# Kernel optimization log

Measured on AMD Instinct MI355X. Metric: run time of the kernel, lower is better.

Reference implementation:

```python
import jax, jax.numpy as jnp
import numpy as np

B, T = 256, 512
DX, DZ, DH1, DH2, DDZ, DDX = 100, 100, 10, 10, 20, 20


def _gru_cell(x, h, W_ih, W_hh, b_ih, b_hh):
    # PyTorch GRU cell: gates ordered (r, z, n)
    gi = x @ W_ih.T + b_ih
    gh = h @ W_hh.T + b_hh
    i_r, i_z, i_n = jnp.split(gi, 3, axis=-1)
    h_r, h_z, h_n = jnp.split(gh, 3, axis=-1)
    r = jax.nn.sigmoid(i_r + h_r)
    u = jax.nn.sigmoid(i_z + h_z)
    n = jnp.tanh(i_n + r * h_n)
    return (1.0 - u) * n + u * h


def _mlp(h_in, W1, b1, Wloc, bloc, Wscale, bscale):
    # stoch_trans: relu hidden -> (loc, softplus scale)
    h = jax.nn.relu(h_in @ W1.T + b1)
    return h @ Wloc.T + bloc, jax.nn.softplus(h @ Wscale.T + bscale)


def setup_inputs() -> dict:
    key = jax.random.key(0)
    ks = jax.random.split(key, 22)
    w = lambda k, s: (jax.random.normal(k, s) * 0.1).astype(jnp.float32)
    return dict(
        x=jax.random.normal(ks[0], (B, T, DX), dtype=jnp.float32),
        eps=jax.random.normal(ks[1], (B, T, DZ), dtype=jnp.float32),
        W_ih1=w(ks[2], (3 * DH1, DZ)), W_hh1=w(ks[3], (3 * DH1, DH1)),
        b_ih1=w(ks[4], (3 * DH1,)), b_hh1=w(ks[5], (3 * DH1,)),
        W_ih2=w(ks[6], (3 * DH2, DX)), W_hh2=w(ks[7], (3 * DH2, DH2)),
        b_ih2=w(ks[8], (3 * DH2,)), b_hh2=w(ks[9], (3 * DH2,)),
        dz_W1=w(ks[10], (DDZ, DH1)), dz_b1=w(ks[11], (DDZ,)),
        dz_Wloc=w(ks[12], (DZ, DDZ)), dz_bloc=w(ks[13], (DZ,)),
        dz_Wscale=w(ks[14], (DZ, DDZ)), dz_bscale=w(ks[15], (DZ,)),
        dx_W1=w(ks[16], (DDX, DH1 + DH2)), dx_b1=w(ks[17], (DDX,)),
        dx_Wloc=w(ks[18], (DX, DDX)), dx_bloc=w(ks[19], (DX,)),
        dx_Wscale=w(ks[20], (DX, DDX)), dx_bscale=w(ks[21], (DX,)),
        h1_0=jnp.zeros((DH1,), jnp.float32),
        h2_0=jnp.zeros((DH2,), jnp.float32),
    )


def reference(x, eps, W_ih1, W_hh1, b_ih1, b_hh1, W_ih2, W_hh2, b_ih2, b_hh2,
              dz_W1, dz_b1, dz_Wloc, dz_bloc, dz_Wscale, dz_bscale,
              dx_W1, dx_b1, dx_Wloc, dx_bloc, dx_Wscale, dx_bscale,
              h1_0, h2_0):
    batch = x.shape[0]
    # gen_RNN_2 over the whole observation sequence (no z dependence -> one scan)
    h2_init = jnp.broadcast_to(h2_0, (batch, DH2))
    def step2(h, xt):
        hn = _gru_cell(xt, h, W_ih2, W_hh2, b_ih2, b_hh2)
        return hn, hn
    _, h2_seq = jax.lax.scan(step2, h2_init, jnp.swapaxes(x, 0, 1))  # (T, B, DH2)
    # dx at step t uses h2 after t-1 inputs; first step uses h2_0
    h2_shift = jnp.concatenate([h2_init[None], h2_seq[:-1]], axis=0)

    # sequential generative rollout: dz MLP -> reparam sample -> gen_RNN_1 step -> dx MLP
    h1_init = jnp.broadcast_to(h1_0, (batch, DH1))
    def step(h1, inp):
        eps_t, h2_t = inp
        z_loc, z_scale = _mlp(h1, dz_W1, dz_b1, dz_Wloc, dz_bloc, dz_Wscale, dz_bscale)
        z_t = z_loc + z_scale * eps_t  # reparameterized Normal sample
        h1n = _gru_cell(z_t, h1, W_ih1, W_hh1, b_ih1, b_hh1)
        x_loc, x_scale = _mlp(jnp.concatenate([h1n, h2_t], axis=-1),
                              dx_W1, dx_b1, dx_Wloc, dx_bloc, dx_Wscale, dx_bscale)
        return h1n, (z_t, z_loc, z_scale, x_loc, x_scale)
    _, outs = jax.lax.scan(step, h1_init, (jnp.swapaxes(eps, 0, 1), h2_shift))
    z_t, z_loc, z_scale, x_loc, x_scale = (jnp.swapaxes(o, 0, 1) for o in outs)
    # (B, T, 2*DX + 3*DZ)
    return jnp.concatenate([x_loc, x_scale, z_loc, z_scale, z_t], axis=-1)
```

## Files before the change

### kernel.cpp

```cpp
#include <hip/hip_runtime.h>

#define NB   256
#define NT   512
#define DHX  100
#define DHZ  100
#define DOUT 500
#define WIN  8
#define RING 16

__device__ __forceinline__ float sgm(float v) { return 1.f / (1.f + __expf(-v)); }
__device__ __forceinline__ float tnh(float v) {
    v = fminf(fmaxf(v, -15.f), 15.f);
    float e = __expf(2.f * v);
    return (e - 1.f) / (e + 1.f);
}
__device__ __forceinline__ float sftp(float v) {
    return fmaxf(v, 0.f) + __logf(1.f + __expf(-fabsf(v)));
}
__device__ __forceinline__ float rdlane(float v, int k) {
    return __uint_as_float(__builtin_amdgcn_readlane(__float_as_uint(v), (unsigned)k));
}

__global__ __launch_bounds__(128, 1) void arfssm(
    const float* __restrict__ x, const float* __restrict__ eps,
    const float* __restrict__ W_ih1, const float* __restrict__ W_hh1,
    const float* __restrict__ b_ih1, const float* __restrict__ b_hh1,
    const float* __restrict__ W_ih2, const float* __restrict__ W_hh2,
    const float* __restrict__ b_ih2, const float* __restrict__ b_hh2,
    const float* __restrict__ dz_W1, const float* __restrict__ dz_b1,
    const float* __restrict__ dz_Wloc, const float* __restrict__ dz_bloc,
    const float* __restrict__ dz_Wscale, const float* __restrict__ dz_bscale,
    const float* __restrict__ dx_W1, const float* __restrict__ dx_b1,
    const float* __restrict__ dx_Wloc, const float* __restrict__ dx_bloc,
    const float* __restrict__ dx_Wscale, const float* __restrict__ dx_bscale,
    const float* __restrict__ h1_0, const float* __restrict__ h2_0,
    float* __restrict__ out)
{
    __shared__ __align__(16) float h1d[RING][12];
    __shared__ __align__(16) float xbuf[2][104];
    __shared__ __align__(16) float zbuf[104];

    const int tid = threadIdx.x;
    const int b   = blockIdx.x;

    if (tid < 64) {
        const int l = tid;

        float wdz1[10]; float bdz1 = 0.f;
        #pragma unroll
        for (int k = 0; k < 10; ++k) wdz1[k] = 0.f;
        if (l < 20) {
            #pragma unroll
            for (int k = 0; k < 10; ++k) wdz1[k] = dz_W1[l * 10 + k];
            bdz1 = dz_b1[l];
        }
        float wzl1[20], wzs1[20];
        #pragma unroll
        for (int k = 0; k < 20; ++k) { wzl1[k] = dz_Wloc[l * 20 + k]; wzs1[k] = dz_Wscale[l * 20 + k]; }
        const float bzl1 = dz_bloc[l], bzs1 = dz_bscale[l];
        float wzl2[20], wzs2[20]; float bzl2 = 0.f, bzs2 = 0.f;
        #pragma unroll
        for (int k = 0; k < 20; ++k) { wzl2[k] = 0.f; wzs2[k] = 0.f; }
        if (l < 36) {
            const int j2 = l + 64;
            #pragma unroll
            for (int k = 0; k < 20; ++k) { wzl2[k] = dz_Wloc[j2 * 20 + k]; wzs2[k] = dz_Wscale[j2 * 20 + k]; }
            bzl2 = dz_bloc[j2]; bzs2 = dz_bscale[j2];
        }
        const int gi_i = l >> 1, gi_h = l & 1;
        float wA[52]; float bih_p = 0.f, bhh_p = 0.f; float whh_p[10];
        #pragma unroll
        for (int k = 0; k < 52; ++k) wA[k] = 0.f;
        #pragma unroll
        for (int k = 0; k < 10; ++k) whh_p[k] = 0.f;
        if (l < 60) {
            const int k0 = gi_h ? 52 : 0;
            const int kn = gi_h ? 48 : 52;
            #pragma unroll
            for (int k = 0; k < 52; ++k) if (k < kn) wA[k] = W_ih1[gi_i * 100 + k0 + k];
            bih_p = b_ih1[gi_i];
            bhh_p = b_hh1[gi_i];
            #pragma unroll
            for (int k = 0; k < 10; ++k) whh_p[k] = W_hh1[gi_i * 10 + k];
        }

        float hs[10];
        #pragma unroll
        for (int k = 0; k < 10; ++k) hs[k] = h1_0[k];
        float h1own = (l < 10) ? h1_0[l] : 0.f;
        if (l < 4) zbuf[100 + l] = 0.f;
        float e1c = eps[(size_t)b * NT * DHZ + l];
        float e2c = (l < 36) ? eps[(size_t)b * NT * DHZ + 64 + l] : 0.f;

        for (int w = 0; w < 64; ++w) {
            #pragma unroll 2
            for (int i = 0; i < 8; ++i) {
                const int t   = 8 * w + i;
                const int wsl = (t + 1) & (RING - 1);

                float hv = bdz1;
                #pragma unroll
                for (int k = 0; k < 10; ++k) hv = fmaf(wdz1[k], hs[k], hv);
                hv = fmaxf(hv, 0.f);
                float hd[20];
                #pragma unroll
                for (int k = 0; k < 20; ++k) hd[k] = rdlane(hv, k);

                const int tn = (t + 1 < NT) ? (t + 1) : t;
                const float* ern = eps + ((size_t)b * NT + tn) * DHZ;
                float e1n = ern[l];
                float e2n = (l < 36) ? ern[64 + l] : 0.f;

                float vl1 = bzl1, vs1 = bzs1, vl2 = bzl2, vs2 = bzs2;
                #pragma unroll
                for (int k = 0; k < 20; ++k) {
                    vl1 = fmaf(wzl1[k], hd[k], vl1); vs1 = fmaf(wzs1[k], hd[k], vs1);
                    vl2 = fmaf(wzl2[k], hd[k], vl2); vs2 = fmaf(wzs2[k], hd[k], vs2);
                }
                float sp1 = sftp(vs1), sp2 = sftp(vs2);
                float zt1 = fmaf(sp1, e1c, vl1);
                float zt2 = fmaf(sp2, e2c, vl2);
                zbuf[l] = zt1;
                if (l < 36) zbuf[64 + l] = zt2;
                __builtin_amdgcn_wave_barrier();

                const size_t ob = ((size_t)b * NT + t) * DOUT;
                out[ob + 200 + l] = vl1; out[ob + 300 + l] = sp1; out[ob + 400 + l] = zt1;
                if (l < 36) { out[ob + 264 + l] = vl2; out[ob + 364 + l] = sp2; out[ob + 464 + l] = zt2; }
                e1c = e1n; e2c = e2n;

                const float4* z4 = (const float4*)zbuf;
                const int b4 = gi_h ? 13 : 0;
                float a0 = 0.f, a1 = 0.f, a2 = 0.f, a3 = 0.f;
                #pragma unroll
                for (int q = 0; q < 13; ++q) {
                    float4 zz = z4[b4 + q];
                    a0 = fmaf(wA[4*q+0], zz.x, a0);
                    a1 = fmaf(wA[4*q+1], zz.y, a1);
                    a2 = fmaf(wA[4*q+2], zz.z, a2);
                    a3 = fmaf(wA[4*q+3], zz.w, a3);
                }
                float acc = (a0 + a1) + (a2 + a3);
                acc += __shfl_xor(acc, 1, 64);
                float gh = bhh_p;
                #pragma unroll
                for (int k = 0; k < 10; ++k) gh = fmaf(whh_p[k], hs[k], gh);
                float gih  = acc + bih_p;
                float gsum = gih + gh;

                float s_r  = __shfl(gsum, 2 * l,      64);
                float s_u  = __shfl(gsum, 2 * l + 20, 64);
                float g_in = __shfl(gih,  2 * l + 40, 64);
                float g_hn = __shfl(gh,   2 * l + 40, 64);
                float r = sgm(s_r), u = sgm(s_u);
                float n = tnh(fmaf(r, g_hn, g_in));
                float h1n_v = (1.f - u) * n + u * h1own;

                if (l < 10) h1d[wsl][l] = h1n_v;
                #pragma unroll
                for (int k = 0; k < 10; ++k) hs[k] = rdlane(h1n_v, k);
                h1own = h1n_v;
            }
            __syncthreads();
        }
        __syncthreads();
    } else {
        const int l = tid - 64;

        float wdx1[20]; float bdx1 = 0.f;
        #pragma unroll
        for (int k = 0; k < 20; ++k) wdx1[k] = 0.f;
        if (l < 20) {
            #pragma unroll
            for (int k = 0; k < 20; ++k) wdx1[k] = dx_W1[l * 20 + k];
            bdx1 = dx_b1[l];
        }
        float wxl1[20], wxs1[20];
        #pragma unroll
        for (int k = 0; k < 20; ++k) { wxl1[k] = dx_Wloc[l * 20 + k]; wxs1[k] = dx_Wscale[l * 20 + k]; }
        const float bxl1 = dx_bloc[l], bxs1 = dx_bscale[l];
        float wxl2[20], wxs2[20]; float bxl2 = 0.f, bxs2 = 0.f;
        #pragma unroll
        for (int k = 0; k < 20; ++k) { wxl2[k] = 0.f; wxs2[k] = 0.f; }
        if (l < 36) {
            const int j2 = l + 64;
            #pragma unroll
            for (int k = 0; k < 20; ++k) { wxl2[k] = dx_Wloc[j2 * 20 + k]; wxs2[k] = dx_Wscale[j2 * 20 + k]; }
            bxl2 = dx_bloc[j2]; bxs2 = dx_bscale[j2];
        }
        const int gi_i = l >> 1, gi_h = l & 1;
        float wB[52]; float bih_p = 0.f, bhh_p = 0.f; float whh_p[10];
        #pragma unroll
        for (int k = 0; k < 52; ++k) wB[k] = 0.f;
        #pragma unroll
        for (int k = 0; k < 10; ++k) whh_p[k] = 0.f;
        if (l < 60) {
            const int k0 = gi_h ? 52 : 0;
            const int kn = gi_h ? 48 : 52;
            #pragma unroll
            for (int k = 0; k < 52; ++k) if (k < kn) wB[k] = W_ih2[gi_i * 100 + k0 + k];
            bih_p = b_ih2[gi_i];
            bhh_p = b_hh2[gi_i];
            #pragma unroll
            for (int k = 0; k < 10; ++k) whh_p[k] = W_hh2[gi_i * 10 + k];
        }

        float hs2[10];
        #pragma unroll
        for (int k = 0; k < 10; ++k) hs2[k] = h2_0[k];
        float h2own = (l < 10) ? h2_0[l] : 0.f;

        if (l < 4) { xbuf[0][100 + l] = 0.f; xbuf[1][100 + l] = 0.f; }
        float4 vh = make_float4(0.f, 0.f, 0.f, 0.f);
        if (l < 25) {
            const float4* xr0 = (const float4*)(x + (size_t)b * NT * DHX);
            const float4* xr1 = (const float4*)(x + ((size_t)b * NT + 1) * DHX);
            float4 v0 = xr0[l];
            vh = xr1[l];
            *((float4*)&xbuf[0][0] + l) = v0;
        }

        __syncthreads();
        for (int w = 1; w < 65; ++w) {
            #pragma unroll 2
            for (int i = 0; i < 8; ++i) {
                const int t = 8 * (w - 1) + i;

                if (l < 25) *((float4*)&xbuf[(t + 1) & 1][0] + l) = vh;
                {
                    const int tn = (t + 2 < NT) ? (t + 2) : (NT - 1);
                    if (l < 25) vh = ((const float4*)(x + ((size_t)b * NT + tn) * DHX))[l];
                }

                const int hsl = (t + 1) & (RING - 1);
                float4 ha = *(const float4*)&h1d[hsl][0];
                float4 hb = *(const float4*)&h1d[hsl][4];
                float h8 = h1d[hsl][8], h9 = h1d[hsl][9];

                const float4* x4 = (const float4*)&xbuf[t & 1][0];
                const int b4 = gi_h ? 13 : 0;
                float a0 = 0.f, a1 = 0.f, a2 = 0.f, a3 = 0.f;
                #pragma unroll
                for (int q = 0; q < 13; ++q) {
                    float4 xx = x4[b4 + q];
                    a0 = fmaf(wB[4*q+0], xx.x, a0);
                    a1 = fmaf(wB[4*q+1], xx.y, a1);
                    a2 = fmaf(wB[4*q+2], xx.z, a2);
                    a3 = fmaf(wB[4*q+3], xx.w, a3);
                }
                float acc = (a0 + a1) + (a2 + a3);
                acc += __shfl_xor(acc, 1, 64);
                float gh = bhh_p;
                #pragma unroll
                for (int k = 0; k < 10; ++k) gh = fmaf(whh_p[k], hs2[k], gh);
                float gih  = acc + bih_p;
                float gsum = gih + gh;
                float s_r  = __shfl(gsum, 2 * l,      64);
                float s_u  = __shfl(gsum, 2 * l + 20, 64);
                float g_in = __shfl(gih,  2 * l + 40, 64);
                float g_hn = __shfl(gh,   2 * l + 40, 64);

                float hv = bdx1;
                hv = fmaf(wdx1[0], ha.x, hv); hv = fmaf(wdx1[1], ha.y, hv);
                hv = fmaf(wdx1[2], ha.z, hv); hv = fmaf(wdx1[3], ha.w, hv);
                hv = fmaf(wdx1[4], hb.x, hv); hv = fmaf(wdx1[5], hb.y, hv);
                hv = fmaf(wdx1[6], hb.z, hv); hv = fmaf(wdx1[7], hb.w, hv);
                hv = fmaf(wdx1[8], h8, hv);   hv = fmaf(wdx1[9], h9, hv);
                #pragma unroll
                for (int k = 0; k < 10; ++k) hv = fmaf(wdx1[10 + k], hs2[k], hv);
                hv = fmaxf(hv, 0.f);
                float hx[20];
                #pragma unroll
                for (int k = 0; k < 20; ++k) hx[k] = rdlane(hv, k);

                float vl1 = bxl1, vs1 = bxs1, vl2 = bxl2, vs2 = bxs2;
                #pragma unroll
                for (int k = 0; k < 20; ++k) {
                    vl1 = fmaf(wxl1[k], hx[k], vl1); vs1 = fmaf(wxs1[k], hx[k], vs1);
                    vl2 = fmaf(wxl2[k], hx[k], vl2); vs2 = fmaf(wxs2[k], hx[k], vs2);
                }
                const size_t ob = ((size_t)b * NT + t) * DOUT;
                out[ob + l]       = vl1;
                out[ob + 100 + l] = sftp(vs1);
                if (l < 36) { out[ob + 64 + l] = vl2; out[ob + 164 + l] = sftp(vs2); }

                float r = sgm(s_r), u = sgm(s_u);
                float n = tnh(fmaf(r, g_hn, g_in));
                float h2n_v = (1.f - u) * n + u * h2own;
                #pragma unroll
                for (int k = 0; k < 10; ++k) hs2[k] = rdlane(h2n_v, k);
                h2own = h2n_v;
            }
            __syncthreads();
        }
    }
}

extern "C" void kernel_launch(void* const* d_in, const int* in_sizes, int n_in,
                              void* d_out, int out_size, void* d_ws, size_t ws_size,
                              hipStream_t stream) {
    (void)in_sizes; (void)n_in; (void)out_size; (void)d_ws; (void)ws_size;
    const float* x         = (const float*)d_in[0];
    const float* eps       = (const float*)d_in[1];
    const float* W_ih1     = (const float*)d_in[2];
    const float* W_hh1     = (const float*)d_in[3];
    const float* b_ih1     = (const float*)d_in[4];
    const float* b_hh1     = (const float*)d_in[5];
    const float* W_ih2     = (const float*)d_in[6];
    const float* W_hh2     = (const float*)d_in[7];
    const float* b_ih2     = (const float*)d_in[8];
    const float* b_hh2     = (const float*)d_in[9];
    const float* dz_W1     = (const float*)d_in[10];
    const float* dz_b1     = (const float*)d_in[11];
    const float* dz_Wloc   = (const float*)d_in[12];
    const float* dz_bloc   = (const float*)d_in[13];
    const float* dz_Wscale = (const float*)d_in[14];
    const float* dz_bscale = (const float*)d_in[15];
    const float* dx_W1     = (const float*)d_in[16];
    const float* dx_b1     = (const float*)d_in[17];
    const float* dx_Wloc   = (const float*)d_in[18];
    const float* dx_bloc   = (const float*)d_in[19];
    const float* dx_Wscale = (const float*)d_in[20];
    const float* dx_bscale = (const float*)d_in[21];
    const float* h1_0      = (const float*)d_in[22];
    const float* h2_0      = (const float*)d_in[23];

    arfssm<<<NB, 128, 0, stream>>>(x, eps, W_ih1, W_hh1, b_ih1, b_hh1,
                                   W_ih2, W_hh2, b_ih2, b_hh2,
                                   dz_W1, dz_b1, dz_Wloc, dz_bloc, dz_Wscale, dz_bscale,
                                   dx_W1, dx_b1, dx_Wloc, dx_bloc, dx_Wscale, dx_bscale,
                                   h1_0, h2_0, (float*)d_out);
}
```

Before: 776.3 us.

## Precompute GRU2 input projections in a separate parallel kernel

Adds a pre-pass kernel that computes x @ W_ih2^T + b_ih2 for all timesteps across many blocks and writes it to workspace. The sequential recurrence wave then only does the small hidden projection and reads the precomputed gates, removing the per-step 100-wide dot product and the x staging buffer from the critical path. It also switches the xor-1 reduction to a DPP swap, hoists the hidden-gate matvec earlier, and uses incrementing pointers. This costs an extra launch plus workspace traffic (about 16 MB written and read).

```diff
diff --git a/kernel.cpp b/kernel.cpp
--- a/kernel.cpp
+++ b/kernel.cpp
@@ -5,8 +5,8 @@
 #define DHX  100
 #define DHZ  100
 #define DOUT 500
-#define WIN  8
 #define RING 16
+#define G2S  32
 
 __device__ __forceinline__ float sgm(float v) { return 1.f / (1.f + __expf(-v)); }
 __device__ __forceinline__ float tnh(float v) {
@@ -20,13 +20,63 @@
 __device__ __forceinline__ float rdlane(float v, int k) {
     return __uint_as_float(__builtin_amdgcn_readlane(__float_as_uint(v), (unsigned)k));
 }
+__device__ __forceinline__ float dpp_xor1_add(float v) {
+    int sw = __builtin_amdgcn_update_dpp(0, __float_as_int(v), 0xB1, 0xF, 0xF, true);
+    return v + __int_as_float(sw);
+}
+
+__global__ __launch_bounds__(256, 1) void gi2_pre(
+    const float* __restrict__ x, const float* __restrict__ W_ih2,
+    const float* __restrict__ b_ih2, float* __restrict__ gi2)
+{
+    const int lane = threadIdx.x & 63;
+    const int wid  = (blockIdx.x << 2) | (threadIdx.x >> 6);
+    const int half = lane >> 5;
+    const int i    = lane & 31;
+
+    float wk[52];
+    #pragma unroll
+    for (int k = 0; k < 52; ++k) wk[k] = 0.f;
+    float bias = 0.f;
+    if (i < 30) {
+        const int k0 = half ? 52 : 0;
+        const int kn = half ? 48 : 52;
+        #pragma unroll
+        for (int k = 0; k < 52; ++k) if (k < kn) wk[k] = W_ih2[i * 100 + k0 + k];
+        bias = b_ih2[i];
+    }
+
+    const int NROW = NB * NT;
+    for (int r = wid; r < NROW; r += 8192) {
+        const float4* x4 = (const float4*)(x + (size_t)r * DHX);
+        const int b4 = half ? 13 : 0;
+        float a0 = 0.f, a1 = 0.f, a2 = 0.f, a3 = 0.f;
+        #pragma unroll
+        for (int q = 0; q < 12; ++q) {
+            float4 v = x4[b4 + q];
+            a0 = fmaf(wk[4*q+0], v.x, a0);
+            a1 = fmaf(wk[4*q+1], v.y, a1);
+            a2 = fmaf(wk[4*q+2], v.z, a2);
+            a3 = fmaf(wk[4*q+3], v.w, a3);
+        }
+        if (!half) {
+            float4 v = x4[12];
+            a0 = fmaf(wk[48], v.x, a0);
+            a1 = fmaf(wk[49], v.y, a1);
+            a2 = fmaf(wk[50], v.z, a2);
+            a3 = fmaf(wk[51], v.w, a3);
+        }
+        float acc = (a0 + a1) + (a2 + a3);
+        acc += __shfl_xor(acc, 32, 64);
+        if (half == 0 && i < 30) gi2[(size_t)r * G2S + i] = acc + bias;
+    }
+}
 
 __global__ __launch_bounds__(128, 1) void arfssm(
-    const float* __restrict__ x, const float* __restrict__ eps,
+    const float* __restrict__ gi2, const float* __restrict__ eps,
     const float* __restrict__ W_ih1, const float* __restrict__ W_hh1,
     const float* __restrict__ b_ih1, const float* __restrict__ b_hh1,
-    const float* __restrict__ W_ih2, const float* __restrict__ W_hh2,
-    const float* __restrict__ b_ih2, const float* __restrict__ b_hh2,
+    const float* __restrict__ W_hh2, const float* __restrict__ b_hh2,
     const float* __restrict__ dz_W1, const float* __restrict__ dz_b1,
     const float* __restrict__ dz_Wloc, const float* __restrict__ dz_bloc,
     const float* __restrict__ dz_Wscale, const float* __restrict__ dz_bscale,
@@ -37,7 +87,6 @@
     float* __restrict__ out)
 {
     __shared__ __align__(16) float h1d[RING][12];
-    __shared__ __align__(16) float xbuf[2][104];
     __shared__ __align__(16) float zbuf[104];
 
     const int tid = threadIdx.x;
@@ -89,8 +138,12 @@
         for (int k = 0; k < 10; ++k) hs[k] = h1_0[k];
         float h1own = (l < 10) ? h1_0[l] : 0.f;
         if (l < 4) zbuf[100 + l] = 0.f;
-        float e1c = eps[(size_t)b * NT * DHZ + l];
-        float e2c = (l < 36) ? eps[(size_t)b * NT * DHZ + 64 + l] : 0.f;
+
+        const float* eprow = eps + (size_t)b * NT * DHZ;
+        float e1c = eprow[l];
+        float e2c = (l < 36) ? eprow[64 + l] : 0.f;
+        eprow += DHZ;
+        float* op0 = out + (size_t)b * NT * DOUT;
 
         for (int w = 0; w < 64; ++w) {
             #pragma unroll 2
@@ -98,6 +151,10 @@
                 const int t   = 8 * w + i;
                 const int wsl = (t + 1) & (RING - 1);
 
+                float gh = bhh_p;
+                #pragma unroll
+                for (int k = 0; k < 10; ++k) gh = fmaf(whh_p[k], hs[k], gh);
+
                 float hv = bdz1;
                 #pragma unroll
                 for (int k = 0; k < 10; ++k) hv = fmaf(wdz1[k], hs[k], hv);
@@ -106,10 +163,8 @@
                 #pragma unroll
                 for (int k = 0; k < 20; ++k) hd[k] = rdlane(hv, k);
 
-                const int tn = (t + 1 < NT) ? (t + 1) : t;
-                const float* ern = eps + ((size_t)b * NT + tn) * DHZ;
-                float e1n = ern[l];
-                float e2n = (l < 36) ? ern[64 + l] : 0.f;
+                float e1n = eprow[l];
+                float e2n = (l < 36) ? eprow[64 + l] : 0.f;
 
                 float vl1 = bzl1, vs1 = bzs1, vl2 = bzl2, vs2 = bzs2;
                 #pragma unroll
@@ -124,9 +179,8 @@
                 if (l < 36) zbuf[64 + l] = zt2;
                 __builtin_amdgcn_wave_barrier();
 
-                const size_t ob = ((size_t)b * NT + t) * DOUT;
-                out[ob + 200 + l] = vl1; out[ob + 300 + l] = sp1; out[ob + 400 + l] = zt1;
-                if (l < 36) { out[ob + 264 + l] = vl2; out[ob + 364 + l] = sp2; out[ob + 464 + l] = zt2; }
+                op0[200 + l] = vl1; op0[300 + l] = sp1; op0[400 + l] = zt1;
+                if (l < 36) { op0[264 + l] = vl2; op0[364 + l] = sp2; op0[464 + l] = zt2; }
                 e1c = e1n; e2c = e2n;
 
                 const float4* z4 = (const float4*)zbuf;
@@ -141,10 +195,7 @@
                     a3 = fmaf(wA[4*q+3], zz.w, a3);
                 }
                 float acc = (a0 + a1) + (a2 + a3);
-                acc += __shfl_xor(acc, 1, 64);
-                float gh = bhh_p;
-                #pragma unroll
-                for (int k = 0; k < 10; ++k) gh = fmaf(whh_p[k], hs[k], gh);
+                acc = dpp_xor1_add(acc);
                 float gih  = acc + bih_p;
                 float gsum = gih + gh;
 
@@ -160,6 +211,9 @@
                 #pragma unroll
                 for (int k = 0; k < 10; ++k) hs[k] = rdlane(h1n_v, k);
                 h1own = h1n_v;
+
+                op0 += DOUT;
+                if (t + 2 < NT) eprow += DHZ;
             }
             __syncthreads();
         }
@@ -188,21 +242,13 @@
             for (int k = 0; k < 20; ++k) { wxl2[k] = dx_Wloc[j2 * 20 + k]; wxs2[k] = dx_Wscale[j2 * 20 + k]; }
             bxl2 = dx_bloc[j2]; bxs2 = dx_bscale[j2];
         }
-        const int gi_i = l >> 1, gi_h = l & 1;
-        float wB[52]; float bih_p = 0.f, bhh_p = 0.f; float whh_p[10];
-        #pragma unroll
-        for (int k = 0; k < 52; ++k) wB[k] = 0.f;
-        #pragma unroll
-        for (int k = 0; k < 10; ++k) whh_p[k] = 0.f;
-        if (l < 60) {
-            const int k0 = gi_h ? 52 : 0;
-            const int kn = gi_h ? 48 : 52;
-            #pragma unroll
-            for (int k = 0; k < 52; ++k) if (k < kn) wB[k] = W_ih2[gi_i * 100 + k0 + k];
-            bih_p = b_ih2[gi_i];
-            bhh_p = b_hh2[gi_i];
-            #pragma unroll
-            for (int k = 0; k < 10; ++k) whh_p[k] = W_hh2[gi_i * 10 + k];
+        float whh2r[10]; float bhh2 = 0.f;
+        #pragma unroll
+        for (int k = 0; k < 10; ++k) whh2r[k] = 0.f;
+        if (l < 30) {
+            #pragma unroll
+            for (int k = 0; k < 10; ++k) whh2r[k] = W_hh2[l * 10 + k];
+            bhh2 = b_hh2[l];
         }
 
         float hs2[10];
@@ -210,15 +256,10 @@
         for (int k = 0; k < 10; ++k) hs2[k] = h2_0[k];
         float h2own = (l < 10) ? h2_0[l] : 0.f;
 
-        if (l < 4) { xbuf[0][100 + l] = 0.f; xbuf[1][100 + l] = 0.f; }
-        float4 vh = make_float4(0.f, 0.f, 0.f, 0.f);
-        if (l < 25) {
-            const float4* xr0 = (const float4*)(x + (size_t)b * NT * DHX);
-            const float4* xr1 = (const float4*)(x + ((size_t)b * NT + 1) * DHX);
-            float4 v0 = xr0[l];
-            vh = xr1[l];
-            *((float4*)&xbuf[0][0] + l) = v0;
-        }
+        const float* g2p = gi2 + (size_t)b * NT * G2S;
+        float gAc = (l < 30) ? g2p[l] : 0.f;
+        g2p += G2S;
+        float* op1 = out + (size_t)b * NT * DOUT;
 
         __syncthreads();
         for (int w = 1; w < 65; ++w) {
@@ -226,39 +267,20 @@
             for (int i = 0; i < 8; ++i) {
                 const int t = 8 * (w - 1) + i;
 
-                if (l < 25) *((float4*)&xbuf[(t + 1) & 1][0] + l) = vh;
-                {
-                    const int tn = (t + 2 < NT) ? (t + 2) : (NT - 1);
-                    if (l < 25) vh = ((const float4*)(x + ((size_t)b * NT + tn) * DHX))[l];
-                }
+                float gAn = (l < 30) ? g2p[l] : 0.f;
 
                 const int hsl = (t + 1) & (RING - 1);
                 float4 ha = *(const float4*)&h1d[hsl][0];
                 float4 hb = *(const float4*)&h1d[hsl][4];
                 float h8 = h1d[hsl][8], h9 = h1d[hsl][9];
 
-                const float4* x4 = (const float4*)&xbuf[t & 1][0];
-                const int b4 = gi_h ? 13 : 0;
-                float a0 = 0.f, a1 = 0.f, a2 = 0.f, a3 = 0.f;
-                #pragma unroll
-                for (int q = 0; q < 13; ++q) {
-                    float4 xx = x4[b4 + q];
-                    a0 = fmaf(wB[4*q+0], xx.x, a0);
-                    a1 = fmaf(wB[4*q+1], xx.y, a1);
-                    a2 = fmaf(wB[4*q+2], xx.z, a2);
-                    a3 = fmaf(wB[4*q+3], xx.w, a3);
-                }
-                float acc = (a0 + a1) + (a2 + a3);
-                acc += __shfl_xor(acc, 1, 64);
-                float gh = bhh_p;
-                #pragma unroll
-                for (int k = 0; k < 10; ++k) gh = fmaf(whh_p[k], hs2[k], gh);
-                float gih  = acc + bih_p;
-                float gsum = gih + gh;
-                float s_r  = __shfl(gsum, 2 * l,      64);
-                float s_u  = __shfl(gsum, 2 * l + 20, 64);
-                float g_in = __shfl(gih,  2 * l + 40, 64);
-                float g_hn = __shfl(gh,   2 * l + 40, 64);
+                float gh = bhh2;
+                #pragma unroll
+                for (int k = 0; k < 10; ++k) gh = fmaf(whh2r[k], hs2[k], gh);
+                float gsum = gAc + gh;
+                float s_u  = __shfl(gsum, l + 10, 64);
+                float g_in = __shfl(gAc,  l + 20, 64);
+                float g_hn = __shfl(gh,   l + 20, 64);
 
                 float hv = bdx1;
                 hv = fmaf(wdx1[0], ha.x, hv); hv = fmaf(wdx1[1], ha.y, hv);
@@ -279,17 +301,21 @@
                     vl1 = fmaf(wxl1[k], hx[k], vl1); vs1 = fmaf(wxs1[k], hx[k], vs1);
                     vl2 = fmaf(wxl2[k], hx[k], vl2); vs2 = fmaf(wxs2[k], hx[k], vs2);
                 }
-                const size_t ob = ((size_t)b * NT + t) * DOUT;
-                out[ob + l]       = vl1;
-                out[ob + 100 + l] = sftp(vs1);
-                if (l < 36) { out[ob + 64 + l] = vl2; out[ob + 164 + l] = sftp(vs2); }
-
-                float r = sgm(s_r), u = sgm(s_u);
+                op1[l]       = vl1;
+                op1[100 + l] = sftp(vs1);
+                if (l < 36) { op1[64 + l] = vl2; op1[164 + l] = sftp(vs2); }
+
+                float r = sgm(gsum);
+                float u = sgm(s_u);
                 float n = tnh(fmaf(r, g_hn, g_in));
                 float h2n_v = (1.f - u) * n + u * h2own;
                 #pragma unroll
                 for (int k = 0; k < 10; ++k) hs2[k] = rdlane(h2n_v, k);
                 h2own = h2n_v;
+
+                op1 += DOUT;
+                gAc = gAn;
+                if (t + 2 < NT) g2p += G2S;
             }
             __syncthreads();
         }
@@ -299,7 +325,7 @@
 extern "C" void kernel_launch(void* const* d_in, const int* in_sizes, int n_in,
                               void* d_out, int out_size, void* d_ws, size_t ws_size,
                               hipStream_t stream) {
-    (void)in_sizes; (void)n_in; (void)out_size; (void)d_ws; (void)ws_size;
+    (void)in_sizes; (void)n_in; (void)out_size; (void)ws_size;
     const float* x         = (const float*)d_in[0];
     const float* eps       = (const float*)d_in[1];
     const float* W_ih1     = (const float*)d_in[2];
@@ -325,8 +351,11 @@
     const float* h1_0      = (const float*)d_in[22];
     const float* h2_0      = (const float*)d_in[23];
 
-    arfssm<<<NB, 128, 0, stream>>>(x, eps, W_ih1, W_hh1, b_ih1, b_hh1,
-                                   W_ih2, W_hh2, b_ih2, b_hh2,
+    float* gi2 = (float*)d_ws;
+
+    gi2_pre<<<2048, 256, 0, stream>>>(x, W_ih2, b_ih2, gi2);
+    arfssm<<<NB, 128, 0, stream>>>(gi2, eps, W_ih1, W_hh1, b_ih1, b_hh1,
+                                   W_hh2, b_hh2,
                                    dz_W1, dz_b1, dz_Wloc, dz_bloc, dz_Wscale, dz_bscale,
                                    dx_W1, dx_b1, dx_Wloc, dx_bloc, dx_Wscale, dx_bscale,
                                    h1_0, h2_0, (float*)d_out);
```

New measurement: 822.1 us. 1.06x slower.
